# Kernel optimization log

Hardware: AMD Instinct MI355X
Metric: run time of the kernel (lower is better)

The kernel has to match this reference:

```python
import jax, jax.numpy as jnp
import numpy as np

EPS = 1e-5

def setup_inputs() -> dict:
    key = jax.random.key(0)
    k1, k2, k3 = jax.random.split(key, 3)
    E, C, OUT = 500000, 64, 128
    x = jax.random.normal(k1, (E, C), dtype=jnp.float32)
    nb = jax.random.randint(k2, (E, 4), 0, E, dtype=jnp.int64)
    W = jax.random.normal(k3, (OUT, 5 * C), dtype=jnp.float32) / np.sqrt(5 * C)
    gamma = jnp.ones((OUT,), dtype=jnp.float32)
    beta = jnp.zeros((OUT,), dtype=jnp.float32)
    return {"x": x, "nb": nb, "W": W, "gamma": gamma, "beta": beta}

def reference(x, nb, W, gamma, beta):
    E, C = x.shape
    idx = jnp.clip(nb, 0, E - 1)          # (E, 4)
    n = x[idx]                             # (E, 4, C) gather
    # pairwise sort (min/max per feature) == torch.sort over a size-2 axis
    p1_lo = jnp.minimum(n[:, 0], n[:, 1])
    p1_hi = jnp.maximum(n[:, 0], n[:, 1])
    p2_lo = jnp.minimum(n[:, 2], n[:, 3])
    p2_hi = jnp.maximum(n[:, 2], n[:, 3])
    feat = jnp.concatenate([x, p1_lo, p1_hi, p2_lo, p2_hi], axis=1)  # (E, 5C)
    h = feat @ W.T                         # (E, out_ch), Linear bias=False
    # BatchNorm1d, training mode: batch mean / biased variance over E
    mean = jnp.mean(h, axis=0)
    var = jnp.mean(jnp.square(h - mean), axis=0)
    h = (h - mean) * (gamma / jnp.sqrt(var + EPS)) + beta
    return jnp.maximum(h, 0.0)             # ReLU
```

## Files before the change

kernel.cpp:

```cpp
#include <hip/hip_runtime.h>
#include <hip/hip_bf16.h>

typedef __attribute__((ext_vector_type(8))) short short8;
typedef __attribute__((ext_vector_type(8))) unsigned short u16x8;
typedef __attribute__((ext_vector_type(4))) float f32x4;

__device__ __forceinline__ unsigned short f2bf(float f) {
    unsigned int u = __float_as_uint(f);
    unsigned int r = (u + 0x7fffu + ((u >> 16) & 1u)) >> 16;
    return (unsigned short)r;
}
__device__ __forceinline__ float bf2f(unsigned short u) {
    return __uint_as_float(((unsigned int)u) << 16);
}
__device__ __forceinline__ float4 min4(float4 a, float4 b) {
    return make_float4(fminf(a.x,b.x), fminf(a.y,b.y), fminf(a.z,b.z), fminf(a.w,b.w));
}
__device__ __forceinline__ float4 max4(float4 a, float4 b) {
    return make_float4(fmaxf(a.x,b.x), fmaxf(a.y,b.y), fmaxf(a.z,b.z), fmaxf(a.w,b.w));
}

__global__ __launch_bounds__(256) void prep_kernel(const float* __restrict__ W,
                                                   unsigned short* __restrict__ Wb,
                                                   float* __restrict__ partials) {
    const int i = blockIdx.x * 256 + threadIdx.x;
    if (i < 64 * 256) partials[i] = 0.f;
    if (i < 128 * 320) Wb[i] = f2bf(W[i]);
}

__global__ __launch_bounds__(256) void prep_conv_kernel(
    const float* __restrict__ W, unsigned short* __restrict__ Wb,
    float* __restrict__ partials,
    const float* __restrict__ x, unsigned short* __restrict__ xb, long n8)
{
    const long g = blockIdx.x * 256L + threadIdx.x;
    if (g < 64 * 256) partials[g] = 0.f;
    if (g < 128 * 320) Wb[g] = f2bf(W[g]);
    const long stride = gridDim.x * 256L;
    for (long i = g; i < n8; i += stride) {
        const f32x4 a = __builtin_nontemporal_load(((const f32x4*)x) + i * 2);
        const f32x4 b = __builtin_nontemporal_load(((const f32x4*)x) + i * 2 + 1);
        u16x8 o;
        o[0] = f2bf(a[0]); o[1] = f2bf(a[1]); o[2] = f2bf(a[2]); o[3] = f2bf(a[3]);
        o[4] = f2bf(b[0]); o[5] = f2bf(b[1]); o[6] = f2bf(b[2]); o[7] = f2bf(b[3]);
        ((u16x8*)xb)[i] = o;
    }
}

template<bool XB, bool BF16H>
__global__ __launch_bounds__(256, 8) void fused_kernel(
    const float* __restrict__ x, const unsigned short* __restrict__ xb,
    const int* __restrict__ nb,
    const unsigned short* __restrict__ Wb, void* __restrict__ hout,
    float* __restrict__ partials, int E)
{
    __shared__ __align__(16) unsigned short feat[32 * 320];

    const int tid = threadIdx.x;
    const int r0 = blockIdx.x * 32;

    {
        const int lr = tid >> 3;
        const int o  = tid & 7;
        const int gr = min(r0 + lr, E - 1);
        int4 nv = *(const int4*)(nb + (long)gr * 4);
        const int i0 = min(max(nv.x, 0), E - 1);
        const int i1 = min(max(nv.y, 0), E - 1);
        const int i2 = min(max(nv.z, 0), E - 1);
        const int i3 = min(max(nv.w, 0), E - 1);
        const int xr = (lr & 7) << 1;
        char* fb = (char*)feat + lr * 640;

        if (XB) {
            const u16x8 xv = *(const u16x8*)(xb + (long)gr * 64 + o * 8);
            const u16x8 av = *(const u16x8*)(xb + (long)i0 * 64 + o * 8);
            const u16x8 bv = *(const u16x8*)(xb + (long)i1 * 64 + o * 8);
            const u16x8 cv = *(const u16x8*)(xb + (long)i2 * 64 + o * 8);
            const u16x8 dv = *(const u16x8*)(xb + (long)i3 * 64 + o * 8);
            u16x8 lo1, hi1, lo2, hi2;
            #pragma unroll
            for (int e = 0; e < 8; ++e) {
                const bool t1 = bf2f(av[e]) < bf2f(bv[e]);
                lo1[e] = t1 ? av[e] : bv[e];
                hi1[e] = t1 ? bv[e] : av[e];
                const bool t2 = bf2f(cv[e]) < bf2f(dv[e]);
                lo2[e] = t2 ? cv[e] : dv[e];
                hi2[e] = t2 ? dv[e] : cv[e];
            }
            const int c8 = o * 2;
            *(u16x8*)(fb + (((c8 +  0) ^ xr) << 3)) = xv;
            *(u16x8*)(fb + (((c8 + 16) ^ xr) << 3)) = lo1;
            *(u16x8*)(fb + (((c8 + 32) ^ xr) << 3)) = hi1;
            *(u16x8*)(fb + (((c8 + 48) ^ xr) << 3)) = lo2;
            *(u16x8*)(fb + (((c8 + 64) ^ xr) << 3)) = hi2;
        } else {
            #pragma unroll
            for (int c = 0; c < 2; ++c) {
                const int col = o * 8 + c * 4;
                const float4 xv = *(const float4*)(x + (long)gr * 64 + col);
                const float4 av = *(const float4*)(x + (long)i0 * 64 + col);
                const float4 bv = *(const float4*)(x + (long)i1 * 64 + col);
                const float4 cv = *(const float4*)(x + (long)i2 * 64 + col);
                const float4 dv = *(const float4*)(x + (long)i3 * 64 + col);
                const float4 vals[5] = { xv, min4(av,bv), max4(av,bv), min4(cv,dv), max4(cv,dv) };
                #pragma unroll
                for (int s = 0; s < 5; ++s) {
                    const int c8 = s * 16 + o * 2 + c;
                    ushort4 p;
                    p.x = f2bf(vals[s].x); p.y = f2bf(vals[s].y);
                    p.z = f2bf(vals[s].z); p.w = f2bf(vals[s].w);
                    *(ushort4*)(fb + ((c8 ^ xr) << 3)) = p;
                }
            }
        }
    }
    __syncthreads();

    const int lane = tid & 63;
    const int wid  = tid >> 6;
    const int lr16 = lane & 15;
    const int lg   = lane >> 4;
    const int xr   = (lr16 & 7) << 1;

    f32x4 acc[2][2];
    #pragma unroll
    for (int m = 0; m < 2; ++m)
        #pragma unroll
        for (int n = 0; n < 2; ++n)
            acc[m][n] = (f32x4){0.f, 0.f, 0.f, 0.f};

    const char* fb0 = (const char*)feat + lr16 * 640;
    const char* fb1 = (const char*)feat + (16 + lr16) * 640;
    const unsigned short* wb = Wb + (wid * 32 + lr16) * 320 + lg * 8;

    #pragma unroll
    for (int kk = 0; kk < 320; kk += 32) {
        const int c8  = (kk >> 2) + lg * 2;
        const int off = (c8 ^ xr) << 3;
        const short8 a0 = *(const short8*)(fb0 + off);
        const short8 a1 = *(const short8*)(fb1 + off);
        const short8 b0 = *(const short8*)(wb + kk);
        const short8 b1 = *(const short8*)(wb + 16 * 320 + kk);
        acc[0][0] = __builtin_amdgcn_mfma_f32_16x16x32_bf16(a0, b0, acc[0][0], 0, 0, 0);
        acc[0][1] = __builtin_amdgcn_mfma_f32_16x16x32_bf16(a0, b1, acc[0][1], 0, 0, 0);
        acc[1][0] = __builtin_amdgcn_mfma_f32_16x16x32_bf16(a1, b0, acc[1][0], 0, 0, 0);
        acc[1][1] = __builtin_amdgcn_mfma_f32_16x16x32_bf16(a1, b1, acc[1][1], 0, 0, 0);
    }

    #pragma unroll
    for (int n = 0; n < 2; ++n) {
        const int col = wid * 32 + n * 16 + lr16;
        float s = 0.f, q = 0.f;
        #pragma unroll
        for (int m = 0; m < 2; ++m) {
            const int rbase = r0 + m * 16 + lg * 4;
            #pragma unroll
            for (int j = 0; j < 4; ++j) {
                if (rbase + j < E) {
                    const float v = acc[m][n][j];
                    s += v;
                    q += v * v;
                }
            }
        }
        s += __shfl_xor(s, 16); s += __shfl_xor(s, 32);
        q += __shfl_xor(q, 16); q += __shfl_xor(q, 32);
        if (lg == 0) {
            float* base = partials + (blockIdx.x & 63) * 256;
            atomicAdd(&base[col], s);
            atomicAdd(&base[128 + col], q);
        }
    }

    if (BF16H) {
        __syncthreads();
        unsigned short* hsm = feat;
        #pragma unroll
        for (int m = 0; m < 2; ++m) {
            const int rb = m * 16 + lg * 4;
            #pragma unroll
            for (int n = 0; n < 2; ++n) {
                const int col = wid * 32 + n * 16 + lr16;
                #pragma unroll
                for (int j = 0; j < 4; ++j)
                    hsm[(rb + j) * 132 + col] = f2bf(acc[m][n][j]);
            }
        }
        __syncthreads();
        unsigned short* hb = (unsigned short*)hout;
        const int oct = tid & 15;
        const int lrr = tid >> 4;
        #pragma unroll
        for (int it = 0; it < 2; ++it) {
            const int r = lrr + it * 16;
            const int grow = r0 + r;
            if (grow < E)
                __builtin_nontemporal_store(
                    *(const u16x8*)(hsm + r * 132 + oct * 8),
                    (u16x8*)(hb + (long)grow * 128 + oct * 8));
        }
    } else {
        float* hf = (float*)hout;
        #pragma unroll
        for (int n = 0; n < 2; ++n) {
            const int col = wid * 32 + n * 16 + lr16;
            #pragma unroll
            for (int m = 0; m < 2; ++m) {
                const int rbase = r0 + m * 16 + lg * 4;
                #pragma unroll
                for (int j = 0; j < 4; ++j) {
                    const int grow = rbase + j;
                    if (grow < E)
                        __builtin_nontemporal_store(acc[m][n][j],
                            hf + (long)grow * 128 + col);
                }
            }
        }
    }
}

__global__ void finalize_kernel(const float* __restrict__ partials,
                                const float* __restrict__ gamma,
                                const float* __restrict__ beta,
                                float* __restrict__ sb, int E)
{
    const int c = threadIdx.x;
    float s = 0.f, q = 0.f;
    for (int b = 0; b < 64; ++b) {
        s += partials[b * 256 + c];
        q += partials[b * 256 + 128 + c];
    }
    const float inv  = 1.0f / (float)E;
    const float mean = s * inv;
    const float var  = fmaxf(q * inv - mean * mean, 0.f);
    const float sc   = gamma[c] / sqrtf(var + 1e-5f);
    sb[c]       = sc;
    sb[128 + c] = beta[c] - mean * sc;
}

__global__ __launch_bounds__(256) void bn_relu_bf16_kernel(
    const unsigned short* __restrict__ hb, const float* __restrict__ sb,
    float* __restrict__ out, long n8)
{
    __shared__ float s_s[128], s_b[128];
    if (threadIdx.x < 128) {
        s_s[threadIdx.x] = sb[threadIdx.x];
        s_b[threadIdx.x] = sb[128 + threadIdx.x];
    }
    __syncthreads();
    long i = blockIdx.x * 256L + threadIdx.x;
    const long stride = gridDim.x * 256L;
    for (; i < n8; i += stride) {
        const u16x8 v = __builtin_nontemporal_load(((const u16x8*)hb) + i);
        const int c0 = ((int)i & 15) << 3;
        f32x4 o0, o1;
        o0[0] = fmaxf(fmaf(bf2f(v[0]), s_s[c0+0], s_b[c0+0]), 0.f);
        o0[1] = fmaxf(fmaf(bf2f(v[1]), s_s[c0+1], s_b[c0+1]), 0.f);
        o0[2] = fmaxf(fmaf(bf2f(v[2]), s_s[c0+2], s_b[c0+2]), 0.f);
        o0[3] = fmaxf(fmaf(bf2f(v[3]), s_s[c0+3], s_b[c0+3]), 0.f);
        o1[0] = fmaxf(fmaf(bf2f(v[4]), s_s[c0+4], s_b[c0+4]), 0.f);
        o1[1] = fmaxf(fmaf(bf2f(v[5]), s_s[c0+5], s_b[c0+5]), 0.f);
        o1[2] = fmaxf(fmaf(bf2f(v[6]), s_s[c0+6], s_b[c0+6]), 0.f);
        o1[3] = fmaxf(fmaf(bf2f(v[7]), s_s[c0+7], s_b[c0+7]), 0.f);
        __builtin_nontemporal_store(o0, ((f32x4*)out) + i * 2);
        __builtin_nontemporal_store(o1, ((f32x4*)out) + i * 2 + 1);
    }
}

__global__ __launch_bounds__(256) void bn_relu_kernel(float* __restrict__ h,
                                                      const float* __restrict__ sb, long n4)
{
    __shared__ float s_s[128], s_b[128];
    if (threadIdx.x < 128) {
        s_s[threadIdx.x] = sb[threadIdx.x];
        s_b[threadIdx.x] = sb[128 + threadIdx.x];
    }
    __syncthreads();
    long i = blockIdx.x * 256L + threadIdx.x;
    const long stride = gridDim.x * 256L;
    for (; i < n4; i += stride) {
        f32x4 v = __builtin_nontemporal_load(((const f32x4*)h) + i);
        const int c = ((int)i * 4) & 127;
        v[0] = fmaxf(fmaf(v[0], s_s[c + 0], s_b[c + 0]), 0.f);
        v[1] = fmaxf(fmaf(v[1], s_s[c + 1], s_b[c + 1]), 0.f);
        v[2] = fmaxf(fmaf(v[2], s_s[c + 2], s_b[c + 2]), 0.f);
        v[3] = fmaxf(fmaf(v[3], s_s[c + 3], s_b[c + 3]), 0.f);
        __builtin_nontemporal_store(v, ((f32x4*)h) + i);
    }
}

extern "C" void kernel_launch(void* const* d_in, const int* in_sizes, int n_in,
                              void* d_out, int out_size, void* d_ws, size_t ws_size,
                              hipStream_t stream)
{
    const float* x     = (const float*)d_in[0];
    const int*   nb    = (const int*)d_in[1];
    const float* W     = (const float*)d_in[2];
    const float* gamma = (const float*)d_in[3];
    const float* beta  = (const float*)d_in[4];
    float* out = (float*)d_out;

    const int E = in_sizes[0] / 64;

    char* ws = (char*)d_ws;
    unsigned short* Wb       = (unsigned short*)ws;
    float*          partials = (float*)(ws + 81920);
    float*          sb       = (float*)(ws + 81920 + 65536);
    unsigned short* xb       = (unsigned short*)(ws + 148480);
    const size_t xb_end = 148480 + (size_t)E * 128;
    unsigned short* hb       = (unsigned short*)(ws + xb_end);
    const bool have_xb = (ws_size >= xb_end);
    const bool have_hb = (ws_size >= xb_end + (size_t)E * 256);

    if (have_xb)
        prep_conv_kernel<<<2048, 256, 0, stream>>>(W, Wb, partials, x, xb, (long)E * 8);
    else
        prep_kernel<<<160, 256, 0, stream>>>(W, Wb, partials);

    const int nblk = (E + 31) / 32;
    void* hdst = have_hb ? (void*)hb : (void*)out;
    if (have_xb && have_hb)
        fused_kernel<true,  true ><<<nblk, 256, 0, stream>>>(x, xb, nb, Wb, hdst, partials, E);
    else if (have_xb)
        fused_kernel<true,  false><<<nblk, 256, 0, stream>>>(x, xb, nb, Wb, hdst, partials, E);
    else if (have_hb)
        fused_kernel<false, true ><<<nblk, 256, 0, stream>>>(x, xb, nb, Wb, hdst, partials, E);
    else
        fused_kernel<false, false><<<nblk, 256, 0, stream>>>(x, xb, nb, Wb, hdst, partials, E);

    finalize_kernel<<<1, 128, 0, stream>>>(partials, gamma, beta, sb, E);

    if (have_hb)
        bn_relu_bf16_kernel<<<2048, 256, 0, stream>>>(hb, sb, out, (long)E * 16);
    else
        bn_relu_kernel<<<2048, 256, 0, stream>>>(out, sb, (long)E * 32);
}
```

Before: 293.9 us.

## Add persistent fused kernel that prefetches next tile's gathered rows

```diff
diff --git a/kernel.cpp b/kernel.cpp
--- a/kernel.cpp
+++ b/kernel.cpp
@@ -47,6 +47,155 @@
     }
 }
 
+__global__ __launch_bounds__(256, 6) void fused_persistent(
+    const unsigned short* __restrict__ xb, const int* __restrict__ nb,
+    const unsigned short* __restrict__ Wb, unsigned short* __restrict__ hb,
+    float* __restrict__ partials, int E, int T)
+{
+    __shared__ __align__(16) unsigned short feat[32 * 320];
+
+    const int tid  = threadIdx.x;
+    const int lr   = tid >> 3;
+    const int o    = tid & 7;
+    const int lane = tid & 63;
+    const int wid  = tid >> 6;
+    const int lr16 = lane & 15;
+    const int lg   = lane >> 4;
+    const int xr_st = (lr & 7) << 1;
+    const int xr_ld = (lr16 & 7) << 1;
+
+    char*       fb_st = (char*)feat + lr * 640;
+    const char* fb0   = (const char*)feat + lr16 * 640;
+    const char* fb1   = (const char*)feat + (16 + lr16) * 640;
+    const unsigned short* wb = Wb + (wid * 32 + lr16) * 320 + lg * 8;
+    float* pbase = partials + (blockIdx.x & 63) * 256;
+
+    u16x8 xv, av, bv, cv, dv;
+
+    int t = blockIdx.x;
+    {
+        const int gr = min(t * 32 + lr, E - 1);
+        int4 nv = *(const int4*)(nb + (long)gr * 4);
+        const int i0 = min(max(nv.x, 0), E - 1);
+        const int i1 = min(max(nv.y, 0), E - 1);
+        const int i2 = min(max(nv.z, 0), E - 1);
+        const int i3 = min(max(nv.w, 0), E - 1);
+        xv = *(const u16x8*)(xb + (long)gr * 64 + o * 8);
+        av = *(const u16x8*)(xb + (long)i0 * 64 + o * 8);
+        bv = *(const u16x8*)(xb + (long)i1 * 64 + o * 8);
+        cv = *(const u16x8*)(xb + (long)i2 * 64 + o * 8);
+        dv = *(const u16x8*)(xb + (long)i3 * 64 + o * 8);
+    }
+
+    for (; t < T; t += gridDim.x) {
+        u16x8 nxv, nav, nbv, ncv, ndv;
+        const int tn = t + gridDim.x;
+        const bool has_next = (tn < T);
+        if (has_next) {
+            const int gr = min(tn * 32 + lr, E - 1);
+            int4 nv = *(const int4*)(nb + (long)gr * 4);
+            const int i0 = min(max(nv.x, 0), E - 1);
+            const int i1 = min(max(nv.y, 0), E - 1);
+            const int i2 = min(max(nv.z, 0), E - 1);
+            const int i3 = min(max(nv.w, 0), E - 1);
+            nxv = *(const u16x8*)(xb + (long)gr * 64 + o * 8);
+            nav = *(const u16x8*)(xb + (long)i0 * 64 + o * 8);
+            nbv = *(const u16x8*)(xb + (long)i1 * 64 + o * 8);
+            ncv = *(const u16x8*)(xb + (long)i2 * 64 + o * 8);
+            ndv = *(const u16x8*)(xb + (long)i3 * 64 + o * 8);
+        }
+
+        {
+            u16x8 lo1, hi1, lo2, hi2;
+            #pragma unroll
+            for (int e = 0; e < 8; ++e) {
+                const bool t1 = bf2f(av[e]) < bf2f(bv[e]);
+                lo1[e] = t1 ? av[e] : bv[e];
+                hi1[e] = t1 ? bv[e] : av[e];
+                const bool t2 = bf2f(cv[e]) < bf2f(dv[e]);
+                lo2[e] = t2 ? cv[e] : dv[e];
+                hi2[e] = t2 ? dv[e] : cv[e];
+            }
+            const int c8 = o * 2;
+            *(u16x8*)(fb_st + (((c8 +  0) ^ xr_st) << 3)) = xv;
+            *(u16x8*)(fb_st + (((c8 + 16) ^ xr_st) << 3)) = lo1;
+            *(u16x8*)(fb_st + (((c8 + 32) ^ xr_st) << 3)) = hi1;
+            *(u16x8*)(fb_st + (((c8 + 48) ^ xr_st) << 3)) = lo2;
+            *(u16x8*)(fb_st + (((c8 + 64) ^ xr_st) << 3)) = hi2;
+        }
+        if (has_next) { xv = nxv; av = nav; bv = nbv; cv = ncv; dv = ndv; }
+        __syncthreads();
+
+        f32x4 acc00 = {0,0,0,0}, acc01 = {0,0,0,0},
+              acc10 = {0,0,0,0}, acc11 = {0,0,0,0};
+        #pragma unroll
+        for (int kk = 0; kk < 320; kk += 32) {
+            const int c8  = (kk >> 2) + lg * 2;
+            const int off = (c8 ^ xr_ld) << 3;
+            const short8 a0 = *(const short8*)(fb0 + off);
+            const short8 a1 = *(const short8*)(fb1 + off);
+            const short8 b0 = *(const short8*)(wb + kk);
+            const short8 b1 = *(const short8*)(wb + 16 * 320 + kk);
+            acc00 = __builtin_amdgcn_mfma_f32_16x16x32_bf16(a0, b0, acc00, 0, 0, 0);
+            acc01 = __builtin_amdgcn_mfma_f32_16x16x32_bf16(a0, b1, acc01, 0, 0, 0);
+            acc10 = __builtin_amdgcn_mfma_f32_16x16x32_bf16(a1, b0, acc10, 0, 0, 0);
+            acc11 = __builtin_amdgcn_mfma_f32_16x16x32_bf16(a1, b1, acc11, 0, 0, 0);
+        }
+
+        const int r0 = t * 32;
+        #pragma unroll
+        for (int n = 0; n < 2; ++n) {
+            const int col = wid * 32 + n * 16 + lr16;
+            float s = 0.f, q = 0.f;
+            #pragma unroll
+            for (int m = 0; m < 2; ++m) {
+                const f32x4& a = (m == 0) ? (n == 0 ? acc00 : acc01)
+                                          : (n == 0 ? acc10 : acc11);
+                const int rbase = r0 + m * 16 + lg * 4;
+                #pragma unroll
+                for (int j = 0; j < 4; ++j) {
+                    if (rbase + j < E) { const float v = a[j]; s += v; q += v * v; }
+                }
+            }
+            s += __shfl_xor(s, 16); s += __shfl_xor(s, 32);
+            q += __shfl_xor(q, 16); q += __shfl_xor(q, 32);
+            if (lg == 0) {
+                atomicAdd(&pbase[col], s);
+                atomicAdd(&pbase[128 + col], q);
+            }
+        }
+        __syncthreads();
+
+        unsigned short* hsm = feat;
+        #pragma unroll
+        for (int m = 0; m < 2; ++m) {
+            const int rb = m * 16 + lg * 4;
+            #pragma unroll
+            for (int n = 0; n < 2; ++n) {
+                const f32x4& a = (m == 0) ? (n == 0 ? acc00 : acc01)
+                                          : (n == 0 ? acc10 : acc11);
+                const int col = wid * 32 + n * 16 + lr16;
+                #pragma unroll
+                for (int j = 0; j < 4; ++j)
+                    hsm[(rb + j) * 132 + col] = f2bf(a[j]);
+            }
+        }
+        __syncthreads();
+        const int oct = tid & 15;
+        const int lrr = tid >> 4;
+        #pragma unroll
+        for (int it = 0; it < 2; ++it) {
+            const int r = lrr + it * 16;
+            const int grow = r0 + r;
+            if (grow < E)
+                __builtin_nontemporal_store(
+                    *(const u16x8*)(hsm + r * 132 + oct * 8),
+                    (u16x8*)(hb + (long)grow * 128 + oct * 8));
+        }
+        __syncthreads();
+    }
+}
+
 template<bool XB, bool BF16H>
 __global__ __launch_bounds__(256, 8) void fused_kernel(
     const float* __restrict__ x, const unsigned short* __restrict__ xb,
@@ -55,10 +204,8 @@
     float* __restrict__ partials, int E)
 {
     __shared__ __align__(16) unsigned short feat[32 * 320];
-
     const int tid = threadIdx.x;
     const int r0 = blockIdx.x * 32;
-
     {
         const int lr = tid >> 3;
         const int o  = tid & 7;
@@ -70,7 +217,6 @@
         const int i3 = min(max(nv.w, 0), E - 1);
         const int xr = (lr & 7) << 1;
         char* fb = (char*)feat + lr * 640;
-
         if (XB) {
             const u16x8 xv = *(const u16x8*)(xb + (long)gr * 64 + o * 8);
             const u16x8 av = *(const u16x8*)(xb + (long)i0 * 64 + o * 8);
@@ -97,12 +243,13 @@
             #pragma unroll
             for (int c = 0; c < 2; ++c) {
                 const int col = o * 8 + c * 4;
-                const float4 xv = *(const float4*)(x + (long)gr * 64 + col);
-                const float4 av = *(const float4*)(x + (long)i0 * 64 + col);
-                const float4 bv = *(const float4*)(x + (long)i1 * 64 + col);
-                const float4 cv = *(const float4*)(x + (long)i2 * 64 + col);
-                const float4 dv = *(const float4*)(x + (long)i3 * 64 + col);
-                const float4 vals[5] = { xv, min4(av,bv), max4(av,bv), min4(cv,dv), max4(cv,dv) };
+                const float4 xvf = *(const float4*)(x + (long)gr * 64 + col);
+                const float4 avf = *(const float4*)(x + (long)i0 * 64 + col);
+                const float4 bvf = *(const float4*)(x + (long)i1 * 64 + col);
+                const float4 cvf = *(const float4*)(x + (long)i2 * 64 + col);
+                const float4 dvf = *(const float4*)(x + (long)i3 * 64 + col);
+                const float4 vals[5] = { xvf, min4(avf,bvf), max4(avf,bvf),
+                                         min4(cvf,dvf), max4(cvf,dvf) };
                 #pragma unroll
                 for (int s = 0; s < 5; ++s) {
                     const int c8 = s * 16 + o * 2 + c;
@@ -115,24 +262,20 @@
         }
     }
     __syncthreads();
-
     const int lane = tid & 63;
     const int wid  = tid >> 6;
     const int lr16 = lane & 15;
     const int lg   = lane >> 4;
     const int xr   = (lr16 & 7) << 1;
-
     f32x4 acc[2][2];
     #pragma unroll
     for (int m = 0; m < 2; ++m)
         #pragma unroll
         for (int n = 0; n < 2; ++n)
             acc[m][n] = (f32x4){0.f, 0.f, 0.f, 0.f};
-
     const char* fb0 = (const char*)feat + lr16 * 640;
     const char* fb1 = (const char*)feat + (16 + lr16) * 640;
     const unsigned short* wb = Wb + (wid * 32 + lr16) * 320 + lg * 8;
-
     #pragma unroll
     for (int kk = 0; kk < 320; kk += 32) {
         const int c8  = (kk >> 2) + lg * 2;
@@ -146,7 +289,6 @@
         acc[1][0] = __builtin_amdgcn_mfma_f32_16x16x32_bf16(a1, b0, acc[1][0], 0, 0, 0);
         acc[1][1] = __builtin_amdgcn_mfma_f32_16x16x32_bf16(a1, b1, acc[1][1], 0, 0, 0);
     }
-
     #pragma unroll
     for (int n = 0; n < 2; ++n) {
         const int col = wid * 32 + n * 16 + lr16;
@@ -158,8 +300,7 @@
             for (int j = 0; j < 4; ++j) {
                 if (rbase + j < E) {
                     const float v = acc[m][n][j];
-                    s += v;
-                    q += v * v;
+                    s += v; q += v * v;
                 }
             }
         }
@@ -171,7 +312,6 @@
             atomicAdd(&base[128 + col], q);
         }
     }
-
     if (BF16H) {
         __syncthreads();
         unsigned short* hsm = feat;
@@ -187,7 +327,7 @@
             }
         }
         __syncthreads();
-        unsigned short* hb = (unsigned short*)hout;
+        unsigned short* hbp = (unsigned short*)hout;
         const int oct = tid & 15;
         const int lrr = tid >> 4;
         #pragma unroll
@@ -197,7 +337,7 @@
             if (grow < E)
                 __builtin_nontemporal_store(
                     *(const u16x8*)(hsm + r * 132 + oct * 8),
-                    (u16x8*)(hb + (long)grow * 128 + oct * 8));
+                    (u16x8*)(hbp + (long)grow * 128 + oct * 8));
         }
     } else {
         float* hf = (float*)hout;
@@ -317,16 +457,17 @@
     else
         prep_kernel<<<160, 256, 0, stream>>>(W, Wb, partials);
 
-    const int nblk = (E + 31) / 32;
-    void* hdst = have_hb ? (void*)hb : (void*)out;
-    if (have_xb && have_hb)
-        fused_kernel<true,  true ><<<nblk, 256, 0, stream>>>(x, xb, nb, Wb, hdst, partials, E);
-    else if (have_xb)
-        fused_kernel<true,  false><<<nblk, 256, 0, stream>>>(x, xb, nb, Wb, hdst, partials, E);
-    else if (have_hb)
-        fused_kernel<false, true ><<<nblk, 256, 0, stream>>>(x, xb, nb, Wb, hdst, partials, E);
-    else
-        fused_kernel<false, false><<<nblk, 256, 0, stream>>>(x, xb, nb, Wb, hdst, partials, E);
+    const int T = (E + 31) / 32;
+    if (have_xb && have_hb) {
+        const int nblk = (T < 1536) ? T : 1536;
+        fused_persistent<<<nblk, 256, 0, stream>>>(xb, nb, Wb, hb, partials, E, T);
+    } else if (have_xb) {
+        fused_kernel<true,  false><<<T, 256, 0, stream>>>(x, xb, nb, Wb, out, partials, E);
+    } else if (have_hb) {
+        fused_kernel<false, true ><<<T, 256, 0, stream>>>(x, xb, nb, Wb, hb, partials, E);
+    } else {
+        fused_kernel<false, false><<<T, 256, 0, stream>>>(x, xb, nb, Wb, out, partials, E);
+    }
 
     finalize_kernel<<<1, 128, 0, stream>>>(partials, gamma, beta, sb, E);
 
```

Measured after the change: 492.0 us. 1.67x slower.

## Add 16-row fused gather-GEMM kernel and widen bf16 BN-ReLU vector width

Applied to the files above, without the earlier changes.

```diff
diff --git a/kernel.cpp b/kernel.cpp
--- a/kernel.cpp
+++ b/kernel.cpp
@@ -47,17 +47,23 @@
     }
 }
 
-template<bool XB, bool BF16H>
-__global__ __launch_bounds__(256, 8) void fused_kernel(
-    const float* __restrict__ x, const unsigned short* __restrict__ xb,
-    const int* __restrict__ nb,
-    const unsigned short* __restrict__ Wb, void* __restrict__ hout,
+__device__ __forceinline__ void bfminmax(unsigned short a, unsigned short b,
+                                         unsigned short& lo, unsigned short& hi) {
+    const float fa = bf2f(a), fb = bf2f(b);
+    lo = (unsigned short)(__float_as_uint(fminf(fa, fb)) >> 16);
+    hi = (unsigned short)(__float_as_uint(fmaxf(fa, fb)) >> 16);
+}
+
+__global__ __launch_bounds__(128, 8) void fused16_kernel(
+    const unsigned short* __restrict__ xb, const int* __restrict__ nb,
+    const unsigned short* __restrict__ Wb, unsigned short* __restrict__ hb,
     float* __restrict__ partials, int E)
 {
-    __shared__ __align__(16) unsigned short feat[32 * 320];
+    __shared__ __align__(16) unsigned short feat[16 * 320];
 
     const int tid = threadIdx.x;
-    const int r0 = blockIdx.x * 32;
+    const int r0 = blockIdx.x * 16;
+    const bool full = (r0 + 16 <= E);
 
     {
         const int lr = tid >> 3;
@@ -71,6 +77,119 @@
         const int xr = (lr & 7) << 1;
         char* fb = (char*)feat + lr * 640;
 
+        const u16x8 xv = *(const u16x8*)(xb + (long)gr * 64 + o * 8);
+        const u16x8 av = *(const u16x8*)(xb + (long)i0 * 64 + o * 8);
+        const u16x8 bv = *(const u16x8*)(xb + (long)i1 * 64 + o * 8);
+        const u16x8 cv = *(const u16x8*)(xb + (long)i2 * 64 + o * 8);
+        const u16x8 dv = *(const u16x8*)(xb + (long)i3 * 64 + o * 8);
+        u16x8 lo1, hi1, lo2, hi2;
+        #pragma unroll
+        for (int e = 0; e < 8; ++e) {
+            unsigned short l, h;
+            bfminmax(av[e], bv[e], l, h); lo1[e] = l; hi1[e] = h;
+            bfminmax(cv[e], dv[e], l, h); lo2[e] = l; hi2[e] = h;
+        }
+        const int c8 = o * 2;
+        *(u16x8*)(fb + (((c8 +  0) ^ xr) << 3)) = xv;
+        *(u16x8*)(fb + (((c8 + 16) ^ xr) << 3)) = lo1;
+        *(u16x8*)(fb + (((c8 + 32) ^ xr) << 3)) = hi1;
+        *(u16x8*)(fb + (((c8 + 48) ^ xr) << 3)) = lo2;
+        *(u16x8*)(fb + (((c8 + 64) ^ xr) << 3)) = hi2;
+    }
+    __syncthreads();
+
+    const int lane = tid & 63;
+    const int w    = tid >> 6;
+    const int lr16 = lane & 15;
+    const int lg   = lane >> 4;
+    const int xr   = (lr16 & 7) << 1;
+    const char* fbA = (const char*)feat + lr16 * 640;
+
+    f32x4 acc[4];
+    #pragma unroll
+    for (int n = 0; n < 4; ++n) acc[n] = (f32x4){0.f, 0.f, 0.f, 0.f};
+
+    #pragma unroll
+    for (int np = 0; np < 2; ++np) {
+        const unsigned short* wb0 = Wb + ((w * 64 + np * 32 + lr16) * 320) + lg * 8;
+        const unsigned short* wb1 = wb0 + 16 * 320;
+        #pragma unroll
+        for (int kk = 0; kk < 320; kk += 32) {
+            const int off = ((((kk >> 2) + lg * 2) ^ xr) << 3);
+            const short8 a  = *(const short8*)(fbA + off);
+            const short8 b0 = *(const short8*)(wb0 + kk);
+            const short8 b1 = *(const short8*)(wb1 + kk);
+            acc[np*2+0] = __builtin_amdgcn_mfma_f32_16x16x32_bf16(a, b0, acc[np*2+0], 0, 0, 0);
+            acc[np*2+1] = __builtin_amdgcn_mfma_f32_16x16x32_bf16(a, b1, acc[np*2+1], 0, 0, 0);
+        }
+    }
+
+    #pragma unroll
+    for (int n = 0; n < 4; ++n) {
+        const int col = w * 64 + n * 16 + lr16;
+        float s = 0.f, q = 0.f;
+        if (full) {
+            #pragma unroll
+            for (int j = 0; j < 4; ++j) { const float v = acc[n][j]; s += v; q += v * v; }
+        } else {
+            #pragma unroll
+            for (int j = 0; j < 4; ++j) {
+                if (r0 + lg * 4 + j < E) { const float v = acc[n][j]; s += v; q += v * v; }
+            }
+        }
+        s += __shfl_xor(s, 16); s += __shfl_xor(s, 32);
+        q += __shfl_xor(q, 16); q += __shfl_xor(q, 32);
+        if (lg == 0) {
+            float* base = partials + (blockIdx.x & 63) * 256;
+            atomicAdd(&base[col], s);
+            atomicAdd(&base[128 + col], q);
+        }
+    }
+
+    __syncthreads();
+    unsigned short* hsm = feat;
+    #pragma unroll
+    for (int n = 0; n < 4; ++n) {
+        const int col = w * 64 + n * 16 + lr16;
+        #pragma unroll
+        for (int j = 0; j < 4; ++j)
+            hsm[(lg * 4 + j) * 132 + col] = f2bf(acc[n][j]);
+    }
+    __syncthreads();
+    const int oct = tid & 15;
+    const int lrr = tid >> 4;
+    #pragma unroll
+    for (int it = 0; it < 2; ++it) {
+        const int r = lrr + it * 8;
+        const int grow = r0 + r;
+        if (full || grow < E)
+            __builtin_nontemporal_store(
+                *(const u16x8*)(hsm + r * 132 + oct * 8),
+                (u16x8*)(hb + (long)grow * 128 + oct * 8));
+    }
+}
+
+template<bool XB, bool BF16H>
+__global__ __launch_bounds__(256, 8) void fused_kernel(
+    const float* __restrict__ x, const unsigned short* __restrict__ xb,
+    const int* __restrict__ nb,
+    const unsigned short* __restrict__ Wb, void* __restrict__ hout,
+    float* __restrict__ partials, int E)
+{
+    __shared__ __align__(16) unsigned short feat[32 * 320];
+    const int tid = threadIdx.x;
+    const int r0 = blockIdx.x * 32;
+    {
+        const int lr = tid >> 3;
+        const int o  = tid & 7;
+        const int gr = min(r0 + lr, E - 1);
+        int4 nv = *(const int4*)(nb + (long)gr * 4);
+        const int i0 = min(max(nv.x, 0), E - 1);
+        const int i1 = min(max(nv.y, 0), E - 1);
+        const int i2 = min(max(nv.z, 0), E - 1);
+        const int i3 = min(max(nv.w, 0), E - 1);
+        const int xr = (lr & 7) << 1;
+        char* fb = (char*)feat + lr * 640;
         if (XB) {
             const u16x8 xv = *(const u16x8*)(xb + (long)gr * 64 + o * 8);
             const u16x8 av = *(const u16x8*)(xb + (long)i0 * 64 + o * 8);
@@ -80,12 +199,9 @@
             u16x8 lo1, hi1, lo2, hi2;
             #pragma unroll
             for (int e = 0; e < 8; ++e) {
-                const bool t1 = bf2f(av[e]) < bf2f(bv[e]);
-                lo1[e] = t1 ? av[e] : bv[e];
-                hi1[e] = t1 ? bv[e] : av[e];
-                const bool t2 = bf2f(cv[e]) < bf2f(dv[e]);
-                lo2[e] = t2 ? cv[e] : dv[e];
-                hi2[e] = t2 ? dv[e] : cv[e];
+                unsigned short l, h;
+                bfminmax(av[e], bv[e], l, h); lo1[e] = l; hi1[e] = h;
+                bfminmax(cv[e], dv[e], l, h); lo2[e] = l; hi2[e] = h;
             }
             const int c8 = o * 2;
             *(u16x8*)(fb + (((c8 +  0) ^ xr) << 3)) = xv;
@@ -97,12 +213,13 @@
             #pragma unroll
             for (int c = 0; c < 2; ++c) {
                 const int col = o * 8 + c * 4;
-                const float4 xv = *(const float4*)(x + (long)gr * 64 + col);
-                const float4 av = *(const float4*)(x + (long)i0 * 64 + col);
-                const float4 bv = *(const float4*)(x + (long)i1 * 64 + col);
-                const float4 cv = *(const float4*)(x + (long)i2 * 64 + col);
-                const float4 dv = *(const float4*)(x + (long)i3 * 64 + col);
-                const float4 vals[5] = { xv, min4(av,bv), max4(av,bv), min4(cv,dv), max4(cv,dv) };
+                const float4 xvf = *(const float4*)(x + (long)gr * 64 + col);
+                const float4 avf = *(const float4*)(x + (long)i0 * 64 + col);
+                const float4 bvf = *(const float4*)(x + (long)i1 * 64 + col);
+                const float4 cvf = *(const float4*)(x + (long)i2 * 64 + col);
+                const float4 dvf = *(const float4*)(x + (long)i3 * 64 + col);
+                const float4 vals[5] = { xvf, min4(avf,bvf), max4(avf,bvf),
+                                         min4(cvf,dvf), max4(cvf,dvf) };
                 #pragma unroll
                 for (int s = 0; s < 5; ++s) {
                     const int c8 = s * 16 + o * 2 + c;
@@ -115,24 +232,20 @@
         }
     }
     __syncthreads();
-
     const int lane = tid & 63;
     const int wid  = tid >> 6;
     const int lr16 = lane & 15;
     const int lg   = lane >> 4;
     const int xr   = (lr16 & 7) << 1;
-
     f32x4 acc[2][2];
     #pragma unroll
     for (int m = 0; m < 2; ++m)
         #pragma unroll
         for (int n = 0; n < 2; ++n)
             acc[m][n] = (f32x4){0.f, 0.f, 0.f, 0.f};
-
     const char* fb0 = (const char*)feat + lr16 * 640;
     const char* fb1 = (const char*)feat + (16 + lr16) * 640;
     const unsigned short* wb = Wb + (wid * 32 + lr16) * 320 + lg * 8;
-
     #pragma unroll
     for (int kk = 0; kk < 320; kk += 32) {
         const int c8  = (kk >> 2) + lg * 2;
@@ -146,7 +259,6 @@
         acc[1][0] = __builtin_amdgcn_mfma_f32_16x16x32_bf16(a1, b0, acc[1][0], 0, 0, 0);
         acc[1][1] = __builtin_amdgcn_mfma_f32_16x16x32_bf16(a1, b1, acc[1][1], 0, 0, 0);
     }
-
     #pragma unroll
     for (int n = 0; n < 2; ++n) {
         const int col = wid * 32 + n * 16 + lr16;
@@ -158,8 +270,7 @@
             for (int j = 0; j < 4; ++j) {
                 if (rbase + j < E) {
                     const float v = acc[m][n][j];
-                    s += v;
-                    q += v * v;
+                    s += v; q += v * v;
                 }
             }
         }
@@ -171,7 +282,6 @@
             atomicAdd(&base[128 + col], q);
         }
     }
-
     if (BF16H) {
         __syncthreads();
         unsigned short* hsm = feat;
@@ -187,7 +297,7 @@
             }
         }
         __syncthreads();
-        unsigned short* hb = (unsigned short*)hout;
+        unsigned short* hbp = (unsigned short*)hout;
         const int oct = tid & 15;
         const int lrr = tid >> 4;
         #pragma unroll
@@ -197,7 +307,7 @@
             if (grow < E)
                 __builtin_nontemporal_store(
                     *(const u16x8*)(hsm + r * 132 + oct * 8),
-                    (u16x8*)(hb + (long)grow * 128 + oct * 8));
+                    (u16x8*)(hbp + (long)grow * 128 + oct * 8));
         }
     } else {
         float* hf = (float*)hout;
@@ -240,7 +350,7 @@
 
 __global__ __launch_bounds__(256) void bn_relu_bf16_kernel(
     const unsigned short* __restrict__ hb, const float* __restrict__ sb,
-    float* __restrict__ out, long n8)
+    float* __restrict__ out, long n16)
 {
     __shared__ float s_s[128], s_b[128];
     if (threadIdx.x < 128) {
@@ -250,20 +360,22 @@
     __syncthreads();
     long i = blockIdx.x * 256L + threadIdx.x;
     const long stride = gridDim.x * 256L;
-    for (; i < n8; i += stride) {
-        const u16x8 v = __builtin_nontemporal_load(((const u16x8*)hb) + i);
-        const int c0 = ((int)i & 15) << 3;
-        f32x4 o0, o1;
-        o0[0] = fmaxf(fmaf(bf2f(v[0]), s_s[c0+0], s_b[c0+0]), 0.f);
-        o0[1] = fmaxf(fmaf(bf2f(v[1]), s_s[c0+1], s_b[c0+1]), 0.f);
-        o0[2] = fmaxf(fmaf(bf2f(v[2]), s_s[c0+2], s_b[c0+2]), 0.f);
-        o0[3] = fmaxf(fmaf(bf2f(v[3]), s_s[c0+3], s_b[c0+3]), 0.f);
-        o1[0] = fmaxf(fmaf(bf2f(v[4]), s_s[c0+4], s_b[c0+4]), 0.f);
-        o1[1] = fmaxf(fmaf(bf2f(v[5]), s_s[c0+5], s_b[c0+5]), 0.f);
-        o1[2] = fmaxf(fmaf(bf2f(v[6]), s_s[c0+6], s_b[c0+6]), 0.f);
-        o1[3] = fmaxf(fmaf(bf2f(v[7]), s_s[c0+7], s_b[c0+7]), 0.f);
-        __builtin_nontemporal_store(o0, ((f32x4*)out) + i * 2);
-        __builtin_nontemporal_store(o1, ((f32x4*)out) + i * 2 + 1);
+    for (; i < n16; i += stride) {
+        const u16x8 v0 = __builtin_nontemporal_load(((const u16x8*)hb) + i * 2);
+        const u16x8 v1 = __builtin_nontemporal_load(((const u16x8*)hb) + i * 2 + 1);
+        const int c0 = ((int)i & 7) << 4;
+        f32x4 o0, o1, o2, o3;
+        #pragma unroll
+        for (int k = 0; k < 4; ++k) {
+            o0[k] = fmaxf(fmaf(bf2f(v0[k]),     s_s[c0+k],      s_b[c0+k]), 0.f);
+            o1[k] = fmaxf(fmaf(bf2f(v0[k+4]),   s_s[c0+4+k],    s_b[c0+4+k]), 0.f);
+            o2[k] = fmaxf(fmaf(bf2f(v1[k]),     s_s[c0+8+k],    s_b[c0+8+k]), 0.f);
+            o3[k] = fmaxf(fmaf(bf2f(v1[k+4]),   s_s[c0+12+k],   s_b[c0+12+k]), 0.f);
+        }
+        __builtin_nontemporal_store(o0, ((f32x4*)out) + i * 4);
+        __builtin_nontemporal_store(o1, ((f32x4*)out) + i * 4 + 1);
+        __builtin_nontemporal_store(o2, ((f32x4*)out) + i * 4 + 2);
+        __builtin_nontemporal_store(o3, ((f32x4*)out) + i * 4 + 3);
     }
 }
 
@@ -317,21 +429,23 @@
     else
         prep_kernel<<<160, 256, 0, stream>>>(W, Wb, partials);
 
-    const int nblk = (E + 31) / 32;
-    void* hdst = have_hb ? (void*)hb : (void*)out;
-    if (have_xb && have_hb)
-        fused_kernel<true,  true ><<<nblk, 256, 0, stream>>>(x, xb, nb, Wb, hdst, partials, E);
-    else if (have_xb)
-        fused_kernel<true,  false><<<nblk, 256, 0, stream>>>(x, xb, nb, Wb, hdst, partials, E);
-    else if (have_hb)
-        fused_kernel<false, true ><<<nblk, 256, 0, stream>>>(x, xb, nb, Wb, hdst, partials, E);
-    else
-        fused_kernel<false, false><<<nblk, 256, 0, stream>>>(x, xb, nb, Wb, hdst, partials, E);
+    if (have_xb && have_hb) {
+        const int T16 = (E + 15) / 16;
+        fused16_kernel<<<T16, 128, 0, stream>>>(xb, nb, Wb, hb, partials, E);
+    } else {
+        const int T = (E + 31) / 32;
+        if (have_xb)
+            fused_kernel<true,  false><<<T, 256, 0, stream>>>(x, xb, nb, Wb, out, partials, E);
+        else if (have_hb)
+            fused_kernel<false, true ><<<T, 256, 0, stream>>>(x, xb, nb, Wb, hb, partials, E);
+        else
+            fused_kernel<false, false><<<T, 256, 0, stream>>>(x, xb, nb, Wb, out, partials, E);
+    }
 
     finalize_kernel<<<1, 128, 0, stream>>>(partials, gamma, beta, sb, E);
 
     if (have_hb)
-        bn_relu_bf16_kernel<<<2048, 256, 0, stream>>>(hb, sb, out, (long)E * 16);
+        bn_relu_bf16_kernel<<<4096, 256, 0, stream>>>(hb, sb, out, (long)E * 8);
     else
         bn_relu_kernel<<<2048, 256, 0, stream>>>(out, sb, (long)E * 32);
 }
```

New measurement: 500.0 us. 70.1% more time.
